# Kernel optimization log

Hardware: AMD Instinct MI355X
Metric: run time of the kernel (lower is better)

The kernel has to match this reference:

```python
import jax, jax.numpy as jnp
import numpy as np

N_NODES = 50000
N_EDGES = 800000
IN_DIM, H1, H2, OUT_DIM = 128, 512, 256, 1


def glorot(key, shape):
    fan_in, fan_out = shape
    lim = jnp.sqrt(6.0 / (fan_in + fan_out))
    return jax.random.uniform(key, shape, jnp.float32, -lim, lim)


def setup_inputs() -> dict:
    key = jax.random.key(0)
    ks = jax.random.split(key, 6)
    x = jax.random.normal(ks[0], (N_NODES, IN_DIM), jnp.float32)
    edge_index = jax.random.randint(ks[1], (2, N_EDGES), 0, N_NODES, jnp.int32)
    edge_attr = jax.random.uniform(ks[2], (N_EDGES,), jnp.float32)
    return {
        "x": x,
        "edge_index": edge_index,
        "edge_attr": edge_attr,
        "W1": glorot(ks[3], (IN_DIM, H1)), "b1": jnp.zeros((H1,), jnp.float32),
        "W2": glorot(ks[4], (H1, H2)), "b2": jnp.zeros((H2,), jnp.float32),
        "W3": glorot(ks[5], (H2, OUT_DIM)), "b3": jnp.zeros((OUT_DIM,), jnp.float32),
    }


def gcn_conv(x, src, dst, ew, W, b, n_nodes):
    # PyG GCNConv with edge weights, normalize=True, add_self_loops=True.
    h = x @ W                                            # [N, F_out]
    # degree includes self-loop weight 1.0 at each node
    deg = jax.ops.segment_sum(ew, dst, num_segments=n_nodes) + 1.0  # [N]
    dis = jnp.where(deg > 0, jax.lax.rsqrt(deg), 0.0)    # deg^{-1/2}
    norm = dis[src] * ew * dis[dst]                      # [E]
    msgs = h[src] * norm[:, None]                        # [E, F_out] gather
    agg = jax.ops.segment_sum(msgs, dst, num_segments=n_nodes)      # scatter-add
    # self-loop contribution: norm_ii = dis_i * 1 * dis_i = 1/deg_i
    agg = agg + h * (dis * dis)[:, None]
    return agg + b


def reference(x, edge_index, edge_attr, W1, b1, W2, b2, W3, b3):
    src, dst = edge_index[0], edge_index[1]
    n = x.shape[0]
    h = jax.nn.relu(gcn_conv(x, src, dst, edge_attr, W1, b1, n))
    h = jax.nn.relu(gcn_conv(h, src, dst, edge_attr, W2, b2, n))
    return gcn_conv(h, src, dst, edge_attr, W3, b3, n)
```

## Files before the change

kernel.cpp:

```cpp
#include <hip/hip_runtime.h>
#include <hip/hip_bf16.h>
#include <stdint.h>

typedef unsigned short u16;
typedef unsigned long long u64;
typedef __attribute__((ext_vector_type(8))) short bf16x8;
typedef __attribute__((ext_vector_type(4))) float f32x4;

constexpr int N_NODES = 50000;
constexpr int N_EDGES = 800000;
constexpr int IN_DIM  = 128;
constexpr int H1_DIM  = 512;
constexpr int H2_DIM  = 256;
constexpr int MT      = 64;
constexpr int MP      = 50048;
constexpr int CAP     = 64;
constexpr int PREP_NB = 3125;

constexpr float DEG_SCALE = 268435456.0f;
constexpr float DEG_INV   = 1.0f / 268435456.0f;

__device__ __forceinline__ u16 f2b(float f) {
  union { float f; unsigned u; } v{f};
  unsigned r = v.u + 0x7fff + ((v.u >> 16) & 1);
  return (u16)(r >> 16);
}
__device__ __forceinline__ float b2f(u16 h) {
  union { unsigned u; float f; } v;
  v.u = ((unsigned)h) << 16;
  return v.f;
}

__device__ __forceinline__ void async16(void* lds, const void* g) {
  __builtin_amdgcn_global_load_lds(
      (const __attribute__((address_space(1))) unsigned int*)g,
      (__attribute__((address_space(3))) unsigned int*)lds, 16, 0, 0);
}

__global__ __launch_bounds__(256) void prep_kernel(
    const int* __restrict__ src, const int* __restrict__ dst,
    const float* __restrict__ ew, u64* __restrict__ degcnt,
    u64* __restrict__ erec,
    const float* __restrict__ W1, u16* __restrict__ w1t,
    const float* __restrict__ W2, u16* __restrict__ w2t) {
  int e = blockIdx.x * 256 + threadIdx.x;
  int d = dst[e];
  int s = src[e];
  float w = ew[e];
  u64 old = atomicAdd(&degcnt[d],
                      ((u64)1 << 40) | (u64)(w * DEG_SCALE + 0.5f));
  if (e < H1_DIM * IN_DIM) {
    int nn = e / IN_DIM, k = e - nn * IN_DIM;
    w1t[e] = f2b(W1[(size_t)k * H1_DIM + nn]);
  }
  if (e < H2_DIM * H1_DIM) {
    int nn = e / H1_DIM, k = e - nn * H1_DIM;
    w2t[e] = f2b(W2[(size_t)k * H2_DIM + nn]);
  }
  int slot = (int)(old >> 40);
  if (slot < CAP)
    erec[(size_t)d * CAP + slot] =
        ((u64)__float_as_uint(w) << 32) | (unsigned)s;
}

__global__ __launch_bounds__(256) void finalize_kernel(
    const u64* __restrict__ degcnt, float* __restrict__ dis,
    int* __restrict__ cnt8, u64* __restrict__ erec,
    const float* __restrict__ x, u16* __restrict__ xb) {
  int t = blockIdx.x * 256 + threadIdx.x;
  int row = t >> 2;
  if (row >= N_NODES) return;
  u64 v = degcnt[row];
  float deg = (float)(v & 0xFFFFFFFFFFULL) * DEG_INV;
  float dr = rsqrtf(deg + 1.0f);
  int q = t & 3;
  if (q == 0) {
    dis[row] = dr;
    int cnt = (int)(v >> 40);
    int c8 = min((cnt + 7) & ~7, CAP);
    cnt8[row] = c8;
    u64* fin = erec + (size_t)row * CAP;
    for (int j = cnt; j < c8; ++j) fin[j] = 0;
  }
  const float* xr = x + (size_t)row * IN_DIM + q * 32;
  u16* xbr = xb + (size_t)row * IN_DIM + q * 32;
#pragma unroll
  for (int k = 0; k < 8; ++k) {
    float4 vx = *(const float4*)(xr + k * 4);
    ushort4 o;
    o.x = f2b(vx.x * dr); o.y = f2b(vx.y * dr);
    o.z = f2b(vx.z * dr); o.w = f2b(vx.w * dr);
    *(ushort4*)(xbr + k * 4) = o;
  }
}

__global__ __launch_bounds__(256) void agg128_kernel(
    const u16* __restrict__ X, const int* __restrict__ cnt8,
    const u64* __restrict__ erec, const float* __restrict__ dis,
    u16* __restrict__ Y) {
  int wid = threadIdx.x >> 6, lane = threadIdx.x & 63;
  int node = __builtin_amdgcn_readfirstlane(blockIdx.x * 4 + wid);
  float dn = dis[node];
  const u16* Xl = X + lane * 2;
  const u64* re = erec + (size_t)node * CAP;
  int c8 = cnt8[node];
  ushort2 sv = *(const ushort2*)(Xl + (size_t)node * 128);
  float a0 = b2f(sv.x), a1 = b2f(sv.y);
  for (int j = 0; j < c8; j += 8) {
    u64 r[8];
#pragma unroll
    for (int q = 0; q < 8; ++q) r[q] = re[j + q];
    ushort2 vv[8];
#pragma unroll
    for (int q = 0; q < 8; ++q)
      vv[q] = *(const ushort2*)(Xl + (size_t)(unsigned)(r[q] & 0xFFFFFFFFu) * 128);
#pragma unroll
    for (int q = 0; q < 8; ++q) {
      float w = __uint_as_float((unsigned)(r[q] >> 32));
      a0 += b2f(vv[q].x) * w;
      a1 += b2f(vv[q].y) * w;
    }
  }
  unsigned pk = ((unsigned)f2b(a1 * dn) << 16) | (unsigned)f2b(a0 * dn);
  *(unsigned*)(Y + (size_t)node * 128 + lane * 2) = pk;
}

__global__ __launch_bounds__(256) void agg256_gemv_kernel(
    const u16* __restrict__ X, const int* __restrict__ cnt8,
    const u64* __restrict__ erec, const float* __restrict__ dis,
    const float* __restrict__ b2, const float* __restrict__ W3,
    float* __restrict__ T2) {
  int wid = threadIdx.x >> 6, lane = threadIdx.x & 63;
  int node = __builtin_amdgcn_readfirstlane(blockIdx.x * 4 + wid);
  float dn = dis[node];
  const u16* Xl = X + lane * 4;
  const u64* re = erec + (size_t)node * CAP;
  int c8 = cnt8[node];
  ushort4 sv = *(const ushort4*)(Xl + (size_t)node * 256);
  float a0 = b2f(sv.x), a1 = b2f(sv.y);
  float a2 = b2f(sv.z), a3 = b2f(sv.w);
  for (int j = 0; j < c8; j += 8) {
    u64 r[8];
#pragma unroll
    for (int q = 0; q < 8; ++q) r[q] = re[j + q];
    ushort4 vv[8];
#pragma unroll
    for (int q = 0; q < 8; ++q)
      vv[q] = *(const ushort4*)(Xl + (size_t)(unsigned)(r[q] & 0xFFFFFFFFu) * 256);
#pragma unroll
    for (int q = 0; q < 8; ++q) {
      float w = __uint_as_float((unsigned)(r[q] >> 32));
      a0 += b2f(vv[q].x) * w;
      a1 += b2f(vv[q].y) * w;
      a2 += b2f(vv[q].z) * w;
      a3 += b2f(vv[q].w) * w;
    }
  }
  float4 bv = *(const float4*)&b2[lane * 4];
  float4 wv = *(const float4*)&W3[lane * 4];
  float s = fmaxf(a0 * dn + bv.x, 0.f) * wv.x + fmaxf(a1 * dn + bv.y, 0.f) * wv.y +
            fmaxf(a2 * dn + bv.z, 0.f) * wv.z + fmaxf(a3 * dn + bv.w, 0.f) * wv.w;
#pragma unroll
  for (int off = 32; off; off >>= 1) s += __shfl_down(s, off);
  if (lane == 0) T2[node] = s * dn;
}

__global__ __launch_bounds__(512, 4) void fused_gemm_kernel(
    const u16* __restrict__ xa, const u16* __restrict__ w1t,
    const u16* __restrict__ w2t, const float* __restrict__ b1,
    const float* __restrict__ dis, u16* __restrict__ t2b, int Mstore) {
  __shared__ u16 xa_s[MT * 128];
  __shared__ u16 h1_s[MT * 128];
  __shared__ u16 ws_s[256 * 64];
  int tid = threadIdx.x;
  int m0 = blockIdx.x * MT;
  int lane = tid & 63, w = tid >> 6;
  int l15 = lane & 15, l4 = lane >> 4;
  int wa = w >> 1;
  int wb = w & 1;

  {
    const char* xb = (const char*)xa + (size_t)m0 * 256;
#pragma unroll
    for (int i = 0; i < 2; ++i) {
      int L = i * 8192 + tid * 16;
      int row = L >> 8;
      int srcoff = (row << 8) + ((L & 255) ^ ((row & 7) << 4));
      async16((char*)xa_s + i * 8192 + (tid & ~63) * 16, xb + srcoff);
    }
  }

  f32x4 acc2[4][2];
#pragma unroll
  for (int i = 0; i < 4; ++i)
#pragma unroll
    for (int j = 0; j < 2; ++j) acc2[i][j] = (f32x4){0.f, 0.f, 0.f, 0.f};

  for (int c = 0; c < 4; ++c) {
    f32x4 acc1[2][2];
#pragma unroll
    for (int i = 0; i < 2; ++i)
#pragma unroll
      for (int j = 0; j < 2; ++j) acc1[i][j] = (f32x4){0.f, 0.f, 0.f, 0.f};

#pragma unroll
    for (int ko = 0; ko < 2; ++ko) {
      {
        const char* wsrc = (const char*)w1t + (size_t)(c * 128) * 256 + ko * 128;
#pragma unroll
        for (int i = 0; i < 2; ++i) {
          int L = i * 8192 + tid * 16;
          int row = L >> 7;
          int srcoff = (row << 8) + ((L & 127) ^ ((row & 7) << 4));
          async16((char*)ws_s + i * 8192 + (tid & ~63) * 16, wsrc + srcoff);
        }
      }
      __syncthreads();
#pragma unroll
      for (int ki = 0; ki < 2; ++ki) {
        bf16x8 a1[2], bx[2];
#pragma unroll
        for (int fn = 0; fn < 2; ++fn) {
          int nr = wa * 32 + fn * 16 + l15;
          int byte = (nr * 128 + ki * 64 + l4 * 16) ^ ((nr & 7) << 4);
          a1[fn] = *(const bf16x8*)((const char*)ws_s + byte);
        }
#pragma unroll
        for (int fm = 0; fm < 2; ++fm) {
          int mr = wb * 32 + fm * 16 + l15;
          int byte = (mr * 256 + ko * 128 + ki * 64 + l4 * 16) ^ ((mr & 7) << 4);
          bx[fm] = *(const bf16x8*)((const char*)xa_s + byte);
        }
#pragma unroll
        for (int fn = 0; fn < 2; ++fn)
#pragma unroll
          for (int fm = 0; fm < 2; ++fm)
            acc1[fn][fm] = __builtin_amdgcn_mfma_f32_16x16x32_bf16(
                a1[fn], bx[fm], acc1[fn][fm], 0, 0, 0);
      }
      __syncthreads();
    }

#pragma unroll
    for (int fn = 0; fn < 2; ++fn) {
      int nloc = wa * 32 + fn * 16 + l4 * 4;
      float4 bv = *(const float4*)&b1[c * 128 + nloc];
#pragma unroll
      for (int fm = 0; fm < 2; ++fm) {
        int mr = wb * 32 + fm * 16 + l15;
        u16 p0 = f2b(fmaxf(acc1[fn][fm][0] + bv.x, 0.f));
        u16 p1 = f2b(fmaxf(acc1[fn][fm][1] + bv.y, 0.f));
        u16 p2 = f2b(fmaxf(acc1[fn][fm][2] + bv.z, 0.f));
        u16 p3 = f2b(fmaxf(acc1[fn][fm][3] + bv.w, 0.f));
        u64 pk = ((u64)p3 << 48) | ((u64)p2 << 32) | ((u64)p1 << 16) | p0;
        int byte = (mr * 256 + nloc * 2) ^ ((mr & 7) << 4);
        *(u64*)((char*)h1_s + byte) = pk;
      }
    }
    __syncthreads();

#pragma unroll
    for (int ko = 0; ko < 2; ++ko) {
      {
        const char* wsrc = (const char*)w2t + (size_t)(c * 128 + ko * 64) * 2;
#pragma unroll
        for (int i = 0; i < 4; ++i) {
          int L = i * 8192 + tid * 16;
          int row = L >> 7;
          int srcoff = row * 1024 + ((L & 127) ^ ((row & 7) << 4));
          async16((char*)ws_s + i * 8192 + (tid & ~63) * 16, wsrc + srcoff);
        }
      }
      __syncthreads();
#pragma unroll
      for (int ki = 0; ki < 2; ++ki) {
        bf16x8 a2[4], bh[2];
#pragma unroll
        for (int fnn = 0; fnn < 4; ++fnn) {
          int nr = wa * 64 + fnn * 16 + l15;
          int byte = (nr * 128 + ki * 64 + l4 * 16) ^ ((nr & 7) << 4);
          a2[fnn] = *(const bf16x8*)((const char*)ws_s + byte);
        }
#pragma unroll
        for (int fm = 0; fm < 2; ++fm) {
          int mr = wb * 32 + fm * 16 + l15;
          int byte = (mr * 256 + ko * 128 + ki * 64 + l4 * 16) ^ ((mr & 7) << 4);
          bh[fm] = *(const bf16x8*)((const char*)h1_s + byte);
        }
#pragma unroll
        for (int fnn = 0; fnn < 4; ++fnn)
#pragma unroll
          for (int fm = 0; fm < 2; ++fm)
            acc2[fnn][fm] = __builtin_amdgcn_mfma_f32_16x16x32_bf16(
                a2[fnn], bh[fm], acc2[fnn][fm], 0, 0, 0);
      }
      __syncthreads();
    }
  }

#pragma unroll
  for (int fnn = 0; fnn < 4; ++fnn) {
    int nn = wa * 64 + fnn * 16 + l4 * 4;
#pragma unroll
    for (int fm = 0; fm < 2; ++fm) {
      int m = m0 + wb * 32 + fm * 16 + l15;
      if (m < Mstore) {
        float dm = dis[m];
        ushort4 pk;
        pk.x = f2b(acc2[fnn][fm][0] * dm);
        pk.y = f2b(acc2[fnn][fm][1] * dm);
        pk.z = f2b(acc2[fnn][fm][2] * dm);
        pk.w = f2b(acc2[fnn][fm][3] * dm);
        *(ushort4*)(t2b + (size_t)m * 256 + nn) = pk;
      }
    }
  }
}

__global__ __launch_bounds__(256) void agg_out_kernel(
    const float* __restrict__ T2, const int* __restrict__ cnt8,
    const u64* __restrict__ erec, const float* __restrict__ dis,
    const float* __restrict__ b3, float* __restrict__ out, int n) {
  const int4* E4 = (const int4*)erec;
  int i = blockIdx.x * 256 + threadIdx.x;
  if (i >= n) return;
  float acc = T2[i];
  int c8 = cnt8[i];
  int h0 = i * (CAP / 2);
  for (int e = 0; e < c8; e += 8) {
    int h = h0 + (e >> 1);
    int4 r0 = E4[h], r1 = E4[h + 1], r2 = E4[h + 2], r3 = E4[h + 3];
    acc += T2[r0.x] * __int_as_float(r0.y) + T2[r0.z] * __int_as_float(r0.w) +
           T2[r1.x] * __int_as_float(r1.y) + T2[r1.z] * __int_as_float(r1.w) +
           T2[r2.x] * __int_as_float(r2.y) + T2[r2.z] * __int_as_float(r2.w) +
           T2[r3.x] * __int_as_float(r3.y) + T2[r3.z] * __int_as_float(r3.w);
  }
  out[i] = acc * dis[i] + b3[0];
}

extern "C" void kernel_launch(void* const* d_in, const int* in_sizes, int n_in,
                              void* d_out, int out_size, void* d_ws, size_t ws_size,
                              hipStream_t stream) {
  const float* x  = (const float*)d_in[0];
  const int*   ei = (const int*)d_in[1];
  const float* ew = (const float*)d_in[2];
  const float* W1 = (const float*)d_in[3];
  const float* b1 = (const float*)d_in[4];
  const float* W2 = (const float*)d_in[5];
  const float* b2 = (const float*)d_in[6];
  const float* W3 = (const float*)d_in[7];
  const float* b3 = (const float*)d_in[8];
  float* out = (float*)d_out;

  const int N = N_NODES, E = N_EDGES;
  const int* src = ei;
  const int* dst = ei + E;

  char* p = (char*)d_ws;
  auto alloc = [&](size_t bytes) -> char* {
    char* r = p;
    p += (bytes + 255) & ~(size_t)255;
    return r;
  };
  u64*   degcnt  = (u64*)  alloc((size_t)N * 8);
  float* dis     = (float*)alloc((size_t)N * 4);
  int*   cnt8    = (int*)  alloc((size_t)N * 4);
  u64*   erec    = (u64*)  alloc((size_t)N * CAP * 8);
  u16*   w1t     = (u16*)  alloc((size_t)H1_DIM * IN_DIM * 2);
  u16*   w2t     = (u16*)  alloc((size_t)H2_DIM * H1_DIM * 2);
  u16*   xb      = (u16*)  alloc((size_t)N * IN_DIM * 2);
  u16*   xa      = (u16*)  alloc((size_t)MP * IN_DIM * 2);
  u16*   t2b     = (u16*)  alloc((size_t)N * H2_DIM * 2);
  float* t3      = (float*)alloc((size_t)N * 4);

  hipMemsetAsync(degcnt, 0, (size_t)N * 8, stream);
  hipMemsetAsync(xa + (size_t)N * IN_DIM, 0, (size_t)(MP - N) * IN_DIM * 2, stream);

  prep_kernel<<<PREP_NB, 256, 0, stream>>>(src, dst, ew, degcnt, erec,
                                           W1, w1t, W2, w2t);

  finalize_kernel<<<(N * 4 + 255) / 256, 256, 0, stream>>>(
      degcnt, dis, cnt8, erec, x, xb);

  agg128_kernel<<<N / 4, 256, 0, stream>>>(xb, cnt8, erec, dis, xa);

  fused_gemm_kernel<<<MP / MT, 512, 0, stream>>>(xa, w1t, w2t, b1, dis, t2b, N);

  agg256_gemv_kernel<<<N / 4, 256, 0, stream>>>(t2b, cnt8, erec, dis, b2, W3, t3);

  agg_out_kernel<<<(N + 255) / 256, 256, 0, stream>>>(t3, cnt8, erec, dis,
                                                      b3, out, N);
}
```

Before: 206.1 us.

## Fuse first-layer aggregation into the fused GEMM kernel prologue

The first-layer neighbor aggregation now runs inside the fused two-GEMM kernel. Each of the 8 waves aggregates 8 nodes and writes the bf16 rows straight into the swizzled shared-memory A tile. This removes the separate aggregation kernel, the global xa buffer round-trip, the padding memset and one launch. The cost is that the gather is now serialized per wave ahead of the MFMA work, with fewer nodes in flight per CU. Latency hiding for the random gathers may therefore suffer.

```diff
diff --git a/kernel.cpp b/kernel.cpp
--- a/kernel.cpp
+++ b/kernel.cpp
@@ -94,35 +94,183 @@
   }
 }
 
-__global__ __launch_bounds__(256) void agg128_kernel(
-    const u16* __restrict__ X, const int* __restrict__ cnt8,
+__global__ __launch_bounds__(512, 4) void agg_gemm_kernel(
+    const u16* __restrict__ xb, const int* __restrict__ cnt8,
     const u64* __restrict__ erec, const float* __restrict__ dis,
-    u16* __restrict__ Y) {
-  int wid = threadIdx.x >> 6, lane = threadIdx.x & 63;
-  int node = __builtin_amdgcn_readfirstlane(blockIdx.x * 4 + wid);
-  float dn = dis[node];
-  const u16* Xl = X + lane * 2;
-  const u64* re = erec + (size_t)node * CAP;
-  int c8 = cnt8[node];
-  ushort2 sv = *(const ushort2*)(Xl + (size_t)node * 128);
-  float a0 = b2f(sv.x), a1 = b2f(sv.y);
-  for (int j = 0; j < c8; j += 8) {
-    u64 r[8];
-#pragma unroll
-    for (int q = 0; q < 8; ++q) r[q] = re[j + q];
-    ushort2 vv[8];
-#pragma unroll
-    for (int q = 0; q < 8; ++q)
-      vv[q] = *(const ushort2*)(Xl + (size_t)(unsigned)(r[q] & 0xFFFFFFFFu) * 128);
-#pragma unroll
-    for (int q = 0; q < 8; ++q) {
-      float w = __uint_as_float((unsigned)(r[q] >> 32));
-      a0 += b2f(vv[q].x) * w;
-      a1 += b2f(vv[q].y) * w;
-    }
-  }
-  unsigned pk = ((unsigned)f2b(a1 * dn) << 16) | (unsigned)f2b(a0 * dn);
-  *(unsigned*)(Y + (size_t)node * 128 + lane * 2) = pk;
+    const u16* __restrict__ w1t, const u16* __restrict__ w2t,
+    const float* __restrict__ b1, u16* __restrict__ t2b, int Mstore) {
+  __shared__ u16 xa_s[MT * 128];
+  __shared__ u16 h1_s[MT * 128];
+  __shared__ u16 ws_s[256 * 64];
+  int tid = threadIdx.x;
+  int m0 = blockIdx.x * MT;
+  int lane = tid & 63, w = tid >> 6;
+  int l15 = lane & 15, l4 = lane >> 4;
+  int wa = w >> 1;
+  int wb = w & 1;
+
+  {
+    const u16* Xl = xb + lane * 2;
+#pragma unroll 1
+    for (int k = 0; k < 8; ++k) {
+      int mloc = w * 8 + k;
+      int node = m0 + mloc;
+      float a0 = 0.f, a1 = 0.f;
+      if (node < Mstore) {
+        float dn = dis[node];
+        ushort2 sv = *(const ushort2*)(Xl + (size_t)node * 128);
+        a0 = b2f(sv.x); a1 = b2f(sv.y);
+        const u64* re = erec + (size_t)node * CAP;
+        int c8 = cnt8[node];
+        for (int j = 0; j < c8; j += 8) {
+          u64 r[8];
+#pragma unroll
+          for (int q = 0; q < 8; ++q) r[q] = re[j + q];
+          ushort2 vv[8];
+#pragma unroll
+          for (int q = 0; q < 8; ++q)
+            vv[q] = *(const ushort2*)(Xl +
+                (size_t)(unsigned)(r[q] & 0xFFFFFFFFu) * 128);
+#pragma unroll
+          for (int q = 0; q < 8; ++q) {
+            float wt = __uint_as_float((unsigned)(r[q] >> 32));
+            a0 += b2f(vv[q].x) * wt;
+            a1 += b2f(vv[q].y) * wt;
+          }
+        }
+        a0 *= dn; a1 *= dn;
+      }
+      unsigned pk = ((unsigned)f2b(a1) << 16) | (unsigned)f2b(a0);
+      int byte = (mloc * 256 + lane * 4) ^ ((mloc & 7) << 4);
+      *(unsigned*)((char*)xa_s + byte) = pk;
+    }
+  }
+
+  f32x4 acc2[4][2];
+#pragma unroll
+  for (int i = 0; i < 4; ++i)
+#pragma unroll
+    for (int j = 0; j < 2; ++j) acc2[i][j] = (f32x4){0.f, 0.f, 0.f, 0.f};
+
+  for (int c = 0; c < 4; ++c) {
+    f32x4 acc1[2][2];
+#pragma unroll
+    for (int i = 0; i < 2; ++i)
+#pragma unroll
+      for (int j = 0; j < 2; ++j) acc1[i][j] = (f32x4){0.f, 0.f, 0.f, 0.f};
+
+#pragma unroll
+    for (int ko = 0; ko < 2; ++ko) {
+      {
+        const char* wsrc = (const char*)w1t + (size_t)(c * 128) * 256 + ko * 128;
+#pragma unroll
+        for (int i = 0; i < 2; ++i) {
+          int L = i * 8192 + tid * 16;
+          int row = L >> 7;
+          int srcoff = (row << 8) + ((L & 127) ^ ((row & 7) << 4));
+          async16((char*)ws_s + i * 8192 + (tid & ~63) * 16, wsrc + srcoff);
+        }
+      }
+      __syncthreads();
+#pragma unroll
+      for (int ki = 0; ki < 2; ++ki) {
+        bf16x8 a1[2], bx[2];
+#pragma unroll
+        for (int fn = 0; fn < 2; ++fn) {
+          int nr = wa * 32 + fn * 16 + l15;
+          int byte = (nr * 128 + ki * 64 + l4 * 16) ^ ((nr & 7) << 4);
+          a1[fn] = *(const bf16x8*)((const char*)ws_s + byte);
+        }
+#pragma unroll
+        for (int fm = 0; fm < 2; ++fm) {
+          int mr = wb * 32 + fm * 16 + l15;
+          int byte = (mr * 256 + ko * 128 + ki * 64 + l4 * 16) ^ ((mr & 7) << 4);
+          bx[fm] = *(const bf16x8*)((const char*)xa_s + byte);
+        }
+#pragma unroll
+        for (int fn = 0; fn < 2; ++fn)
+#pragma unroll
+          for (int fm = 0; fm < 2; ++fm)
+            acc1[fn][fm] = __builtin_amdgcn_mfma_f32_16x16x32_bf16(
+                a1[fn], bx[fm], acc1[fn][fm], 0, 0, 0);
+      }
+      __syncthreads();
+    }
+
+#pragma unroll
+    for (int fn = 0; fn < 2; ++fn) {
+      int nloc = wa * 32 + fn * 16 + l4 * 4;
+      float4 bv = *(const float4*)&b1[c * 128 + nloc];
+#pragma unroll
+      for (int fm = 0; fm < 2; ++fm) {
+        int mr = wb * 32 + fm * 16 + l15;
+        u16 p0 = f2b(fmaxf(acc1[fn][fm][0] + bv.x, 0.f));
+        u16 p1 = f2b(fmaxf(acc1[fn][fm][1] + bv.y, 0.f));
+        u16 p2 = f2b(fmaxf(acc1[fn][fm][2] + bv.z, 0.f));
+        u16 p3 = f2b(fmaxf(acc1[fn][fm][3] + bv.w, 0.f));
+        u64 pk = ((u64)p3 << 48) | ((u64)p2 << 32) | ((u64)p1 << 16) | p0;
+        int byte = (mr * 256 + nloc * 2) ^ ((mr & 7) << 4);
+        *(u64*)((char*)h1_s + byte) = pk;
+      }
+    }
+    __syncthreads();
+
+#pragma unroll
+    for (int ko = 0; ko < 2; ++ko) {
+      {
+        const char* wsrc = (const char*)w2t + (size_t)(c * 128 + ko * 64) * 2;
+#pragma unroll
+        for (int i = 0; i < 4; ++i) {
+          int L = i * 8192 + tid * 16;
+          int row = L >> 7;
+          int srcoff = row * 1024 + ((L & 127) ^ ((row & 7) << 4));
+          async16((char*)ws_s + i * 8192 + (tid & ~63) * 16, wsrc + srcoff);
+        }
+      }
+      __syncthreads();
+#pragma unroll
+      for (int ki = 0; ki < 2; ++ki) {
+        bf16x8 a2[4], bh[2];
+#pragma unroll
+        for (int fnn = 0; fnn < 4; ++fnn) {
+          int nr = wa * 64 + fnn * 16 + l15;
+          int byte = (nr * 128 + ki * 64 + l4 * 16) ^ ((nr & 7) << 4);
+          a2[fnn] = *(const bf16x8*)((const char*)ws_s + byte);
+        }
+#pragma unroll
+        for (int fm = 0; fm < 2; ++fm) {
+          int mr = wb * 32 + fm * 16 + l15;
+          int byte = (mr * 256 + ko * 128 + ki * 64 + l4 * 16) ^ ((mr & 7) << 4);
+          bh[fm] = *(const bf16x8*)((const char*)h1_s + byte);
+        }
+#pragma unroll
+        for (int fnn = 0; fnn < 4; ++fnn)
+#pragma unroll
+          for (int fm = 0; fm < 2; ++fm)
+            acc2[fnn][fm] = __builtin_amdgcn_mfma_f32_16x16x32_bf16(
+                a2[fnn], bh[fm], acc2[fnn][fm], 0, 0, 0);
+      }
+      __syncthreads();
+    }
+  }
+
+#pragma unroll
+  for (int fnn = 0; fnn < 4; ++fnn) {
+    int nn = wa * 64 + fnn * 16 + l4 * 4;
+#pragma unroll
+    for (int fm = 0; fm < 2; ++fm) {
+      int m = m0 + wb * 32 + fm * 16 + l15;
+      if (m < Mstore) {
+        float dm = dis[m];
+        ushort4 pk;
+        pk.x = f2b(acc2[fnn][fm][0] * dm);
+        pk.y = f2b(acc2[fnn][fm][1] * dm);
+        pk.z = f2b(acc2[fnn][fm][2] * dm);
+        pk.w = f2b(acc2[fnn][fm][3] * dm);
+        *(ushort4*)(t2b + (size_t)m * 256 + nn) = pk;
+      }
+    }
+  }
 }
 
 __global__ __launch_bounds__(256) void agg256_gemv_kernel(
@@ -163,158 +311,6 @@
 #pragma unroll
   for (int off = 32; off; off >>= 1) s += __shfl_down(s, off);
   if (lane == 0) T2[node] = s * dn;
-}
-
-__global__ __launch_bounds__(512, 4) void fused_gemm_kernel(
-    const u16* __restrict__ xa, const u16* __restrict__ w1t,
-    const u16* __restrict__ w2t, const float* __restrict__ b1,
-    const float* __restrict__ dis, u16* __restrict__ t2b, int Mstore) {
-  __shared__ u16 xa_s[MT * 128];
-  __shared__ u16 h1_s[MT * 128];
-  __shared__ u16 ws_s[256 * 64];
-  int tid = threadIdx.x;
-  int m0 = blockIdx.x * MT;
-  int lane = tid & 63, w = tid >> 6;
-  int l15 = lane & 15, l4 = lane >> 4;
-  int wa = w >> 1;
-  int wb = w & 1;
-
-  {
-    const char* xb = (const char*)xa + (size_t)m0 * 256;
-#pragma unroll
-    for (int i = 0; i < 2; ++i) {
-      int L = i * 8192 + tid * 16;
-      int row = L >> 8;
-      int srcoff = (row << 8) + ((L & 255) ^ ((row & 7) << 4));
-      async16((char*)xa_s + i * 8192 + (tid & ~63) * 16, xb + srcoff);
-    }
-  }
-
-  f32x4 acc2[4][2];
-#pragma unroll
-  for (int i = 0; i < 4; ++i)
-#pragma unroll
-    for (int j = 0; j < 2; ++j) acc2[i][j] = (f32x4){0.f, 0.f, 0.f, 0.f};
-
-  for (int c = 0; c < 4; ++c) {
-    f32x4 acc1[2][2];
-#pragma unroll
-    for (int i = 0; i < 2; ++i)
-#pragma unroll
-      for (int j = 0; j < 2; ++j) acc1[i][j] = (f32x4){0.f, 0.f, 0.f, 0.f};
-
-#pragma unroll
-    for (int ko = 0; ko < 2; ++ko) {
-      {
-        const char* wsrc = (const char*)w1t + (size_t)(c * 128) * 256 + ko * 128;
-#pragma unroll
-        for (int i = 0; i < 2; ++i) {
-          int L = i * 8192 + tid * 16;
-          int row = L >> 7;
-          int srcoff = (row << 8) + ((L & 127) ^ ((row & 7) << 4));
-          async16((char*)ws_s + i * 8192 + (tid & ~63) * 16, wsrc + srcoff);
-        }
-      }
-      __syncthreads();
-#pragma unroll
-      for (int ki = 0; ki < 2; ++ki) {
-        bf16x8 a1[2], bx[2];
-#pragma unroll
-        for (int fn = 0; fn < 2; ++fn) {
-          int nr = wa * 32 + fn * 16 + l15;
-          int byte = (nr * 128 + ki * 64 + l4 * 16) ^ ((nr & 7) << 4);
-          a1[fn] = *(const bf16x8*)((const char*)ws_s + byte);
-        }
-#pragma unroll
-        for (int fm = 0; fm < 2; ++fm) {
-          int mr = wb * 32 + fm * 16 + l15;
-          int byte = (mr * 256 + ko * 128 + ki * 64 + l4 * 16) ^ ((mr & 7) << 4);
-          bx[fm] = *(const bf16x8*)((const char*)xa_s + byte);
-        }
-#pragma unroll
-        for (int fn = 0; fn < 2; ++fn)
-#pragma unroll
-          for (int fm = 0; fm < 2; ++fm)
-            acc1[fn][fm] = __builtin_amdgcn_mfma_f32_16x16x32_bf16(
-                a1[fn], bx[fm], acc1[fn][fm], 0, 0, 0);
-      }
-      __syncthreads();
-    }
-
-#pragma unroll
-    for (int fn = 0; fn < 2; ++fn) {
-      int nloc = wa * 32 + fn * 16 + l4 * 4;
-      float4 bv = *(const float4*)&b1[c * 128 + nloc];
-#pragma unroll
-      for (int fm = 0; fm < 2; ++fm) {
-        int mr = wb * 32 + fm * 16 + l15;
-        u16 p0 = f2b(fmaxf(acc1[fn][fm][0] + bv.x, 0.f));
-        u16 p1 = f2b(fmaxf(acc1[fn][fm][1] + bv.y, 0.f));
-        u16 p2 = f2b(fmaxf(acc1[fn][fm][2] + bv.z, 0.f));
-        u16 p3 = f2b(fmaxf(acc1[fn][fm][3] + bv.w, 0.f));
-        u64 pk = ((u64)p3 << 48) | ((u64)p2 << 32) | ((u64)p1 << 16) | p0;
-        int byte = (mr * 256 + nloc * 2) ^ ((mr & 7) << 4);
-        *(u64*)((char*)h1_s + byte) = pk;
-      }
-    }
-    __syncthreads();
-
-#pragma unroll
-    for (int ko = 0; ko < 2; ++ko) {
-      {
-        const char* wsrc = (const char*)w2t + (size_t)(c * 128 + ko * 64) * 2;
-#pragma unroll
-        for (int i = 0; i < 4; ++i) {
-          int L = i * 8192 + tid * 16;
-          int row = L >> 7;
-          int srcoff = row * 1024 + ((L & 127) ^ ((row & 7) << 4));
-          async16((char*)ws_s + i * 8192 + (tid & ~63) * 16, wsrc + srcoff);
-        }
-      }
-      __syncthreads();
-#pragma unroll
-      for (int ki = 0; ki < 2; ++ki) {
-        bf16x8 a2[4], bh[2];
-#pragma unroll
-        for (int fnn = 0; fnn < 4; ++fnn) {
-          int nr = wa * 64 + fnn * 16 + l15;
-          int byte = (nr * 128 + ki * 64 + l4 * 16) ^ ((nr & 7) << 4);
-          a2[fnn] = *(const bf16x8*)((const char*)ws_s + byte);
-        }
-#pragma unroll
-        for (int fm = 0; fm < 2; ++fm) {
-          int mr = wb * 32 + fm * 16 + l15;
-          int byte = (mr * 256 + ko * 128 + ki * 64 + l4 * 16) ^ ((mr & 7) << 4);
-          bh[fm] = *(const bf16x8*)((const char*)h1_s + byte);
-        }
-#pragma unroll
-        for (int fnn = 0; fnn < 4; ++fnn)
-#pragma unroll
-          for (int fm = 0; fm < 2; ++fm)
-            acc2[fnn][fm] = __builtin_amdgcn_mfma_f32_16x16x32_bf16(
-                a2[fnn], bh[fm], acc2[fnn][fm], 0, 0, 0);
-      }
-      __syncthreads();
-    }
-  }
-
-#pragma unroll
-  for (int fnn = 0; fnn < 4; ++fnn) {
-    int nn = wa * 64 + fnn * 16 + l4 * 4;
-#pragma unroll
-    for (int fm = 0; fm < 2; ++fm) {
-      int m = m0 + wb * 32 + fm * 16 + l15;
-      if (m < Mstore) {
-        float dm = dis[m];
-        ushort4 pk;
-        pk.x = f2b(acc2[fnn][fm][0] * dm);
-        pk.y = f2b(acc2[fnn][fm][1] * dm);
-        pk.z = f2b(acc2[fnn][fm][2] * dm);
-        pk.w = f2b(acc2[fnn][fm][3] * dm);
-        *(ushort4*)(t2b + (size_t)m * 256 + nn) = pk;
-      }
-    }
-  }
 }
 
 __global__ __launch_bounds__(256) void agg_out_kernel(
@@ -369,12 +365,10 @@
   u16*   w1t     = (u16*)  alloc((size_t)H1_DIM * IN_DIM * 2);
   u16*   w2t     = (u16*)  alloc((size_t)H2_DIM * H1_DIM * 2);
   u16*   xb      = (u16*)  alloc((size_t)N * IN_DIM * 2);
-  u16*   xa      = (u16*)  alloc((size_t)MP * IN_DIM * 2);
   u16*   t2b     = (u16*)  alloc((size_t)N * H2_DIM * 2);
   float* t3      = (float*)alloc((size_t)N * 4);
 
   hipMemsetAsync(degcnt, 0, (size_t)N * 8, stream);
-  hipMemsetAsync(xa + (size_t)N * IN_DIM, 0, (size_t)(MP - N) * IN_DIM * 2, stream);
 
   prep_kernel<<<PREP_NB, 256, 0, stream>>>(src, dst, ew, degcnt, erec,
                                            W1, w1t, W2, w2t);
@@ -382,9 +376,8 @@
   finalize_kernel<<<(N * 4 + 255) / 256, 256, 0, stream>>>(
       degcnt, dis, cnt8, erec, x, xb);
 
-  agg128_kernel<<<N / 4, 256, 0, stream>>>(xb, cnt8, erec, dis, xa);
-
-  fused_gemm_kernel<<<MP / MT, 512, 0, stream>>>(xa, w1t, w2t, b1, dis, t2b, N);
+  agg_gemm_kernel<<<MP / MT, 512, 0, stream>>>(xb, cnt8, erec, dis,
+                                               w1t, w2t, b1, t2b, N);
 
   agg256_gemv_kernel<<<N / 4, 256, 0, stream>>>(t2b, cnt8, erec, dis, b2, W3, t3);
 
```

New measurement: 212.8 us. 3.3% more time.
